# Kernel optimization log

Hardware: AMD Instinct MI355X
Metric: run time of the kernel (lower is better)

## Reference

```python
import jax, jax.numpy as jnp
import numpy as np

P = 256        # number of graph pairs
LMAX = 32      # max graph size (padded to LMAX+1 incl. virtual node)
F = 2048       # num_input_features
E = 256        # embedding_dim
INF = 10000.0


def _lengths():
    i = np.arange(P)
    len_s = 8 + (i % 25)
    len_t = 8 + ((7 * i + 3) % 25)
    return len_s.astype(np.int32), len_t.astype(np.int32)


def setup_inputs() -> dict:
    key = jax.random.key(0)
    ks = jax.random.split(key, 6)
    len_s_np, len_t_np = _lengths()
    Ns, Nt = int(len_s_np.sum()), int(len_t_np.sum())
    x_s = jax.random.normal(ks[0], (Ns, F), jnp.float32)
    x_t = jax.random.normal(ks[1], (Nt, F), jnp.float32)
    W1 = jax.random.normal(ks[2], (E, F), jnp.float32) / np.float32(np.sqrt(F))
    b1 = jnp.zeros((E,), jnp.float32)
    W2 = jax.random.normal(ks[3], (E, E), jnp.float32) / np.float32(np.sqrt(E))
    b2 = jnp.zeros((E,), jnp.float32)
    virtual_embedding = jax.random.uniform(ks[4], (F,), jnp.float32)
    return {"x_s": x_s, "x_t": x_t, "W1": W1, "b1": b1, "W2": W2, "b2": b2,
            "virtual_embedding": virtual_embedding,
            "len_s": jnp.asarray(len_s_np), "len_t": jnp.asarray(len_t_np)}


def _embed(x, W1, b1, W2, b2):
    # nn.Sequential(Linear, Dropout(eval=identity), ReLU, Linear, ReLU)
    h = jax.nn.relu(x @ W1.T + b1)
    return jax.nn.relu(h @ W2.T + b2)


def _safe_cdist(a, b):
    # a: [P,L,E], b: [P,L,E] -> [P,L,L] Euclidean, grad-safe at 0
    sq = (jnp.sum(a * a, -1)[:, :, None] + jnp.sum(b * b, -1)[:, None, :]
          - 2.0 * jnp.einsum('pid,pjd->pij', a, b))
    sq = jnp.maximum(sq, 0.0)
    pos = sq > 0
    return jnp.where(pos, jnp.sqrt(jnp.where(pos, sq, 1.0)), 0.0)


def _pad_embed(emb, virtual_e, lens):
    # ragged [N,E] -> padded [P,LMAX+1,E]; slot lens[p] (and beyond) = virtual
    pos = jnp.arange(LMAX + 1)
    off = jnp.cumsum(lens) - lens                       # exclusive prefix sum
    idx = off[:, None] + jnp.minimum(pos[None, :], lens[:, None] - 1)
    mask = pos[None, :] < lens[:, None]
    return jnp.where(mask[..., None], emb[idx], virtual_e[None, None, :])


def _edit_costs(x_s, x_t, W1, b1, W2, b2, virtual_embedding, len_s, len_t):
    emb_s = _embed(x_s, W1, b1, W2, b2)
    emb_t = _embed(x_t, W1, b1, W2, b2)
    ve = _embed(virtual_embedding[None, :], W1, b1, W2, b2)[0]
    A = _pad_embed(emb_s, ve, len_s)                    # [P,L+1,E]
    B = _pad_embed(emb_t, ve, len_t)
    d = _safe_cdist(A, B)                               # [P,L+1,L+1]
    pos = jnp.arange(LMAX + 1)
    valid = ((pos[None, :, None] <= len_s[:, None, None]) &
             (pos[None, None, :] <= len_t[:, None, None]))
    tot = jnp.sum(jnp.where(valid, d, 0.0), axis=(1, 2))
    scale = (len_s * len_t).astype(d.dtype) / tot
    return jnp.where(valid, d * scale[:, None, None], 0.0), valid


def _lap_jv(C):
    # Jonker-Volgenant / e-maxx Hungarian for square cost matrix; returns col of each row
    C = np.asarray(C, dtype=np.float64)
    n = C.shape[0]
    u = np.zeros(n + 1)
    v = np.zeros(n + 1)
    p = np.zeros(n + 1, dtype=np.int64)
    way = np.zeros(n + 1, dtype=np.int64)
    for i in range(1, n + 1):
        p[0] = i
        j0 = 0
        minv = np.full(n + 1, np.inf)
        used = np.zeros(n + 1, dtype=bool)
        while True:
            used[j0] = True
            i0 = p[j0]
            cur = C[i0 - 1, :] - u[i0] - v[1:]
            upd = (~used[1:]) & (cur < minv[1:])
            minv[1:][upd] = cur[upd]
            way[1:][upd] = j0
            masked = np.where(used[1:], np.inf, minv[1:])
            j1 = int(np.argmin(masked)) + 1
            delta = masked[j1 - 1]
            u[p[used]] += delta
            v[used] -= delta
            minv[1:][~used[1:]] -= delta
            j0 = j1
            if p[j0] == 0:
                break
        while j0:
            j1 = way[j0]
            p[j0] = p[j1]
            j0 = j1
    row_of_col = p[1:] - 1
    col_of_row = np.empty(n, dtype=np.int64)
    col_of_row[row_of_col] = np.arange(n)
    return col_of_row


def _lsape_align(ec, n, m):
    # LSAPE expansion identical to GEDModelHomology.lsape
    N = n + m
    C = np.zeros((N, N))
    C[:n, :m] = ec[:n, :m]
    C[n:, :m] = INF
    C[:n, m:] = INF
    C[np.arange(n, n + m), np.arange(m)] = ec[n, :m]
    C[np.arange(n), np.arange(m, m + n)] = ec[:n, m]
    C[~np.isfinite(C)] = INF
    p = _lap_jv(C)
    q = np.arange(N)
    align = np.zeros((n + 1, m + 1), dtype=np.int32)
    align[np.minimum(q, n), np.minimum(p, m)] = 1
    align[-1, -1] = 0
    return align


def _alignments(costs_np, len_s_np, len_t_np):
    out = np.zeros((costs_np.shape[0], LMAX + 1, LMAX + 1), dtype=np.int32)
    for pr in range(costs_np.shape[0]):
        n, m = int(len_s_np[pr]), int(len_t_np[pr])
        out[pr, :n + 1, :m + 1] = _lsape_align(costs_np[pr, :n + 1, :m + 1], n, m)
    return out


def reference(x_s, x_t, W1, b1, W2, b2, virtual_embedding, len_s, len_t):
    costs, _ = _edit_costs(x_s, x_t, W1, b1, W2, b2, virtual_embedding, len_s, len_t)
    aligns = jnp.asarray(_alignments(np.asarray(costs),
                                     np.asarray(len_s), np.asarray(len_t)))
    geds = (jnp.sum(aligns.astype(costs.dtype) * costs, axis=(1, 2))
            / (len_s + len_t).astype(costs.dtype))
    return aligns, costs, geds
```

## Files before the change

kernel.cpp:

```cpp
#include <hip/hip_runtime.h>
#include <math.h>

#define LMAXP1 33
#define EDIM   256
#define FBIG   3.0e38f

typedef _Float16 half8 __attribute__((ext_vector_type(8)));
typedef float    f32x4 __attribute__((ext_vector_type(4)));

__device__ inline unsigned pk2h(_Float16 a, _Float16 b) {
    union { _Float16 h[2]; unsigned u; } q; q.h[0] = a; q.h[1] = b; return q.u;
}

__global__ __launch_bounds__(256)
void k_convw(const float* __restrict__ W, unsigned* __restrict__ Wh,
             unsigned* __restrict__ Wl, int npairs, float scale) {
    const int stride = gridDim.x * blockDim.x;
    for (int i = blockIdx.x * blockDim.x + threadIdx.x; i < npairs; i += stride) {
        const float a0 = W[2*i] * scale, a1 = W[2*i+1] * scale;
        const _Float16 h0 = (_Float16)a0, h1 = (_Float16)a1;
        const _Float16 l0 = (_Float16)(a0 - (float)h0);
        const _Float16 l1 = (_Float16)(a1 - (float)h1);
        Wh[i] = pk2h(h0, h1); Wl[i] = pk2h(l0, l1);
    }
}

__global__ __launch_bounds__(256)
void k_norms(const unsigned* __restrict__ Eh, const unsigned* __restrict__ El,
             float* __restrict__ Norms, int Mtot) {
    const int row  = blockIdx.x * 4 + (threadIdx.x >> 6);
    const int lane = threadIdx.x & 63;
    if (row >= Mtot) return;
    const uint2 h2 = *(const uint2*)(Eh + (size_t)row * 128 + lane * 2);
    const uint2 l2 = *(const uint2*)(El + (size_t)row * 128 + lane * 2);
    union { unsigned u; _Float16 h[2]; } qh, ql;
    float s = 0.f;
    qh.u = h2.x; ql.u = l2.x;
    { const float x0 = (float)qh.h[0] + (float)ql.h[0];
      const float x1 = (float)qh.h[1] + (float)ql.h[1];
      s = fmaf(x0, x0, s); s = fmaf(x1, x1, s); }
    qh.u = h2.y; ql.u = l2.y;
    { const float x0 = (float)qh.h[0] + (float)ql.h[0];
      const float x1 = (float)qh.h[1] + (float)ql.h[1];
      s = fmaf(x0, x0, s); s = fmaf(x1, x1, s); }
    #pragma unroll
    for (int off = 32; off > 0; off >>= 1) s += __shfl_xor(s, off);
    if (lane == 0) Norms[row] = s;
}

#define ASTR 20
__global__ __launch_bounds__(256)
void k_gemm_splitk(const float* __restrict__ S0, int n0,
                   const float* __restrict__ S1, int n1,
                   const float* __restrict__ S2,
                   const unsigned* __restrict__ Wh, const unsigned* __restrict__ Wl,
                   float* __restrict__ Part, int Mtot, int K, int kchunk) {
    __shared__ alignas(16) unsigned AsH[64 * ASTR],  AsL[64 * ASTR];
    __shared__ alignas(16) unsigned BsH[128 * ASTR], BsL[128 * ASTR];
    const int tid = threadIdx.x;
    const int m0  = blockIdx.x * 64;
    const int nc0 = blockIdx.y * 128;
    const int ks  = blockIdx.z;
    const int kb  = ks * kchunk;
    const int ke  = (kb + kchunk < K) ? kb + kchunk : K;

    const int sar = tid >> 2, sak = (tid & 3) << 3;
    const int gr  = m0 + sar;
    const float* srow = nullptr;
    if (gr < n0)            srow = S0 + (size_t)gr * K;
    else if (gr < n0 + n1)  srow = S1 + (size_t)(gr - n0) * K;
    else if (gr < Mtot)     srow = S2;

    const int lane = tid & 63, wv = tid >> 6;
    const int wc = wv << 5;
    const int lr = lane & 15, lq = lane >> 4;

    f32x4 acc[4][2] = {};

    for (int k0 = kb; k0 < ke; k0 += 32) {
        {
            float x[8];
            if (srow) {
                const float4 f0 = *(const float4*)(srow + k0 + sak + 0);
                const float4 f1 = *(const float4*)(srow + k0 + sak + 4);
                x[0]=f0.x; x[1]=f0.y; x[2]=f0.z; x[3]=f0.w;
                x[4]=f1.x; x[5]=f1.y; x[6]=f1.z; x[7]=f1.w;
            } else {
                #pragma unroll
                for (int j = 0; j < 8; ++j) x[j] = 0.f;
            }
            unsigned uh[4], ul[4];
            #pragma unroll
            for (int j = 0; j < 4; ++j) {
                const _Float16 h0 = (_Float16)x[2*j],   h1 = (_Float16)x[2*j+1];
                const _Float16 l0 = (_Float16)(x[2*j]   - (float)h0);
                const _Float16 l1 = (_Float16)(x[2*j+1] - (float)h1);
                uh[j] = pk2h(h0, h1); ul[j] = pk2h(l0, l1);
            }
            *(uint4*)(AsH + sar * ASTR + (sak >> 1)) = make_uint4(uh[0],uh[1],uh[2],uh[3]);
            *(uint4*)(AsL + sar * ASTR + (sak >> 1)) = make_uint4(ul[0],ul[1],ul[2],ul[3]);
        }
        #pragma unroll
        for (int it = 0; it < 2; ++it) {
            const int idx = tid + it * 256;
            const int br = idx >> 2, bk = (idx & 3) << 3;
            const size_t uoff = (size_t)(nc0 + br) * (K >> 1) + ((k0 + bk) >> 1);
            *(uint4*)(BsH + br * ASTR + (bk >> 1)) = *(const uint4*)(Wh + uoff);
            *(uint4*)(BsL + br * ASTR + (bk >> 1)) = *(const uint4*)(Wl + uoff);
        }
        __syncthreads();

        half8 bhv[2], blv[2];
        #pragma unroll
        for (int ct = 0; ct < 2; ++ct) {
            const int br = wc + ct * 16 + lr;
            bhv[ct] = *(const half8*)((const char*)BsH + br * 80 + lq * 16);
            blv[ct] = *(const half8*)((const char*)BsL + br * 80 + lq * 16);
        }
        #pragma unroll
        for (int rt = 0; rt < 4; ++rt) {
            const int ar = rt * 16 + lr;
            const half8 ah = *(const half8*)((const char*)AsH + ar * 80 + lq * 16);
            const half8 al = *(const half8*)((const char*)AsL + ar * 80 + lq * 16);
            #pragma unroll
            for (int ct = 0; ct < 2; ++ct) {
                acc[rt][ct] = __builtin_amdgcn_mfma_f32_16x16x32_f16(ah, bhv[ct], acc[rt][ct], 0, 0, 0);
                acc[rt][ct] = __builtin_amdgcn_mfma_f32_16x16x32_f16(ah, blv[ct], acc[rt][ct], 0, 0, 0);
                acc[rt][ct] = __builtin_amdgcn_mfma_f32_16x16x32_f16(al, bhv[ct], acc[rt][ct], 0, 0, 0);
            }
        }
        __syncthreads();
    }

    float* pout = Part + (size_t)ks * ((size_t)Mtot * EDIM);
    const float sc = 1.0f / 1024.0f;
    #pragma unroll
    for (int rt = 0; rt < 4; ++rt) {
        #pragma unroll
        for (int r = 0; r < 4; ++r) {
            const int grr = m0 + rt * 16 + lq * 4 + r;
            if (grr >= Mtot) continue;
            #pragma unroll
            for (int ct = 0; ct < 2; ++ct)
                pout[(size_t)grr * EDIM + nc0 + wc + ct * 16 + lr] = acc[rt][ct][r] * sc;
        }
    }
}

__global__ __launch_bounds__(256)
void k_reduce_bias_relu(const float* __restrict__ Part,
                        const float* __restrict__ bias,
                        unsigned* __restrict__ Hh, unsigned* __restrict__ Hl,
                        int S, size_t MN4) {
    const size_t i = (size_t)blockIdx.x * blockDim.x + threadIdx.x;
    const size_t stride = (size_t)gridDim.x * blockDim.x;
    const size_t MN = MN4 * 4;
    for (size_t i4 = i; i4 < MN4; i4 += stride) {
        float4 s = ((const float4*)Part)[i4];
        for (int z = 1; z < S; ++z)
            { const float4 q = ((const float4*)(Part + (size_t)z * MN))[i4];
              s.x += q.x; s.y += q.y; s.z += q.z; s.w += q.w; }
        const float4 b = ((const float4*)bias)[i4 & 63];
        s.x = fmaxf(s.x + b.x, 0.f); s.y = fmaxf(s.y + b.y, 0.f);
        s.z = fmaxf(s.z + b.z, 0.f); s.w = fmaxf(s.w + b.w, 0.f);
        const _Float16 hx = (_Float16)s.x, hy = (_Float16)s.y;
        const _Float16 hz = (_Float16)s.z, hw = (_Float16)s.w;
        Hh[i4*2+0] = pk2h(hx, hy);
        Hh[i4*2+1] = pk2h(hz, hw);
        Hl[i4*2+0] = pk2h((_Float16)(s.x - (float)hx), (_Float16)(s.y - (float)hy));
        Hl[i4*2+1] = pk2h((_Float16)(s.z - (float)hz), (_Float16)(s.w - (float)hw));
    }
}

__global__ __launch_bounds__(256)
void k_gemm_f16(const unsigned* __restrict__ Ah, const unsigned* __restrict__ Al,
                const unsigned* __restrict__ Wh, const unsigned* __restrict__ Wl,
                const float* __restrict__ bias,
                unsigned* __restrict__ Eh, unsigned* __restrict__ El,
                int Mtot, int K) {
    __shared__ alignas(16) unsigned AsH[64 * ASTR],  AsL[64 * ASTR];
    __shared__ alignas(16) unsigned BsH[256 * ASTR], BsL[256 * ASTR];
    const int tid = threadIdx.x;
    const int m0  = blockIdx.x * 64;

    const int sar = tid >> 2, sak = (tid & 3) << 3;
    const int gr  = m0 + sar;
    const bool arow = (gr < Mtot);

    const int lane = tid & 63, wv = tid >> 6;
    const int wc = wv << 6;
    const int lr = lane & 15, lq = lane >> 4;

    f32x4 acc[4][4] = {};

    for (int k0 = 0; k0 < K; k0 += 32) {
        {
            uint4 vh = make_uint4(0,0,0,0), vl = vh;
            if (arow) {
                const size_t uoff = (size_t)gr * (K >> 1) + ((k0 + sak) >> 1);
                vh = *(const uint4*)(Ah + uoff);
                vl = *(const uint4*)(Al + uoff);
            }
            *(uint4*)(AsH + sar * ASTR + (sak >> 1)) = vh;
            *(uint4*)(AsL + sar * ASTR + (sak >> 1)) = vl;
        }
        #pragma unroll
        for (int it = 0; it < 4; ++it) {
            const int idx = tid + it * 256;
            const int br = idx >> 2, bk = (idx & 3) << 3;
            const size_t uoff = (size_t)br * (K >> 1) + ((k0 + bk) >> 1);
            *(uint4*)(BsH + br * ASTR + (bk >> 1)) = *(const uint4*)(Wh + uoff);
            *(uint4*)(BsL + br * ASTR + (bk >> 1)) = *(const uint4*)(Wl + uoff);
        }
        __syncthreads();

        half8 bhv[4], blv[4];
        #pragma unroll
        for (int ct = 0; ct < 4; ++ct) {
            const int br = wc + ct * 16 + lr;
            bhv[ct] = *(const half8*)((const char*)BsH + br * 80 + lq * 16);
            blv[ct] = *(const half8*)((const char*)BsL + br * 80 + lq * 16);
        }
        #pragma unroll
        for (int rt = 0; rt < 4; ++rt) {
            const int ar = rt * 16 + lr;
            const half8 ah = *(const half8*)((const char*)AsH + ar * 80 + lq * 16);
            const half8 al = *(const half8*)((const char*)AsL + ar * 80 + lq * 16);
            #pragma unroll
            for (int ct = 0; ct < 4; ++ct) {
                acc[rt][ct] = __builtin_amdgcn_mfma_f32_16x16x32_f16(ah, bhv[ct], acc[rt][ct], 0, 0, 0);
                acc[rt][ct] = __builtin_amdgcn_mfma_f32_16x16x32_f16(ah, blv[ct], acc[rt][ct], 0, 0, 0);
                acc[rt][ct] = __builtin_amdgcn_mfma_f32_16x16x32_f16(al, bhv[ct], acc[rt][ct], 0, 0, 0);
            }
        }
        __syncthreads();
    }

    _Float16* ph = (_Float16*)Eh;
    _Float16* pl = (_Float16*)El;
    const float sc = 1.0f / 1024.0f;
    #pragma unroll
    for (int rt = 0; rt < 4; ++rt) {
        #pragma unroll
        for (int r = 0; r < 4; ++r) {
            const int grr = m0 + rt * 16 + lq * 4 + r;
            if (grr >= Mtot) continue;
            #pragma unroll
            for (int ct = 0; ct < 4; ++ct) {
                const int gc = wc + ct * 16 + lr;
                const float vv = fmaxf(acc[rt][ct][r] * sc + bias[gc], 0.0f);
                const _Float16 hv = (_Float16)vv;
                ph[(size_t)grr * EDIM + gc] = hv;
                pl[(size_t)grr * EDIM + gc] = (_Float16)(vv - (float)hv);
            }
        }
    }
}

__global__ __launch_bounds__(256)
void k_embed_gemm(const float* __restrict__ S0, int n0,
                  const float* __restrict__ S1, int n1,
                  const float* __restrict__ S2,
                  const float* __restrict__ W, const float* __restrict__ bias,
                  float* __restrict__ C, int Mtot, int K) {
    __shared__ alignas(16) float As[16][68];
    __shared__ alignas(16) float Bs[16][68];
    const int tid  = threadIdx.x;
    const int tx   = tid & 15, ty = tid >> 4;
    const int m0   = blockIdx.x * 64, nc0 = blockIdx.y * 64;
    const int lrow = tid >> 2;
    const int lk4  = (tid & 3) << 2;

    const int gr = m0 + lrow;
    const float* srow = nullptr;
    if (gr < n0)            srow = S0 + (size_t)gr * K;
    else if (gr < n0 + n1)  srow = S1 + (size_t)(gr - n0) * K;
    else if (gr < Mtot)     srow = S2;
    const float* wrow = W + (size_t)(nc0 + lrow) * K;

    float acc[4][4] = {};
    for (int k0 = 0; k0 < K; k0 += 16) {
        float4 va = make_float4(0.f, 0.f, 0.f, 0.f);
        if (srow) va = *(const float4*)(srow + k0 + lk4);
        const float4 vb = *(const float4*)(wrow + k0 + lk4);
        As[lk4+0][lrow] = va.x; As[lk4+1][lrow] = va.y;
        As[lk4+2][lrow] = va.z; As[lk4+3][lrow] = va.w;
        Bs[lk4+0][lrow] = vb.x; Bs[lk4+1][lrow] = vb.y;
        Bs[lk4+2][lrow] = vb.z; Bs[lk4+3][lrow] = vb.w;
        __syncthreads();
        #pragma unroll
        for (int kk = 0; kk < 16; ++kk) {
            const float4 a4 = *(const float4*)&As[kk][ty << 2];
            const float4 b4 = *(const float4*)&Bs[kk][tx << 2];
            const float av[4] = {a4.x, a4.y, a4.z, a4.w};
            const float bv[4] = {b4.x, b4.y, b4.z, b4.w};
            #pragma unroll
            for (int i2 = 0; i2 < 4; ++i2)
                #pragma unroll
                for (int j2 = 0; j2 < 4; ++j2)
                    acc[i2][j2] = fmaf(av[i2], bv[j2], acc[i2][j2]);
        }
        __syncthreads();
    }
    #pragma unroll
    for (int i2 = 0; i2 < 4; ++i2) {
        const int grr = m0 + (ty << 2) + i2;
        if (grr >= Mtot) continue;
        #pragma unroll
        for (int j2 = 0; j2 < 4; ++j2) {
            const int gc = nc0 + (tx << 2) + j2;
            const float vv = acc[i2][j2] + bias[gc];
            C[(size_t)grr * EDIM + gc] = fmaxf(vv, 0.0f);
        }
    }
}

#define CSTR 36
__global__ __launch_bounds__(256)
void k_costs(const unsigned* __restrict__ Eh, const unsigned* __restrict__ El,
             const float* __restrict__ Norms,
             const int* __restrict__ len_s, const int* __restrict__ len_t,
             int Ns, int Nt, float* __restrict__ costs) {
    __shared__ alignas(16) unsigned Ah[34 * CSTR], Al[34 * CSTR];
    __shared__ alignas(16) unsigned Bh[34 * CSTR], Bl[34 * CSTR];
    __shared__ float dtile[LMAXP1 * LMAXP1];
    __shared__ float na[LMAXP1], nb[LMAXP1];
    __shared__ float red[256];
    __shared__ float s_scale;
    const int p = blockIdx.x, tid = threadIdx.x;
    const int n = len_s[p], m = len_t[p];
    int offs = 0, offt = 0;
    for (int j = 0; j < p; ++j) { offs += len_s[j]; offt += len_t[j]; }
    const int veRow = Ns + Nt;
    const int tbase = Ns + offt;

    const int lane = tid & 63, wv = tid >> 6;
    const int lr = lane & 15, lq = lane >> 4;

    if (tid <= n)                       na[tid] = Norms[(tid < n) ? offs + tid : veRow];
    else if (tid >= 64 && tid - 64 <= m) nb[tid - 64] = Norms[(tid - 64 < m) ? tbase + tid - 64 : veRow];

    f32x4 g0 = {}, g1 = {}, g2 = {};
    const int t0 = wv, t1 = wv + 4, t2 = wv + 8;

    for (int k0 = 0; k0 < EDIM; k0 += 64) {
        for (int idx = tid; idx < 34 * 16; idx += 256) {
            const int r = idx >> 4, c4 = idx & 15;
            const int rowA = (r < n) ? offs + r : ((r == n) ? veRow : -1);
            const int rowB = (r < m) ? tbase + r : ((r == m) ? veRow : -1);
            uint2 vah = make_uint2(0,0), val = vah, vbh = vah, vbl = vah;
            if (rowA >= 0) {
                const size_t uo_ = (size_t)rowA * 128 + (k0 >> 1) + c4 * 2;
                vah = *(const uint2*)(Eh + uo_); val = *(const uint2*)(El + uo_);
            }
            if (rowB >= 0) {
                const size_t uo_ = (size_t)rowB * 128 + (k0 >> 1) + c4 * 2;
                vbh = *(const uint2*)(Eh + uo_); vbl = *(const uint2*)(El + uo_);
            }
            const int uo = r * CSTR + c4 * 2;
            *(uint2*)(Ah + uo) = vah; *(uint2*)(Al + uo) = val;
            *(uint2*)(Bh + uo) = vbh; *(uint2*)(Bl + uo) = vbl;
        }
        __syncthreads();

        #pragma unroll
        for (int kf = 0; kf < 2; ++kf) {
#define GRAM_TILE(T, G) { \
            const int tr_ = (T) / 3, tc_ = (T) % 3;                              \
            const int ar_ = tr_ * 16 + lr, br_ = tc_ * 16 + lr;                  \
            const half8 ah = *(const half8*)((const char*)Ah + ar_*144 + kf*64 + lq*16); \
            const half8 al = *(const half8*)((const char*)Al + ar_*144 + kf*64 + lq*16); \
            const half8 bh = *(const half8*)((const char*)Bh + br_*144 + kf*64 + lq*16); \
            const half8 bl = *(const half8*)((const char*)Bl + br_*144 + kf*64 + lq*16); \
            G = __builtin_amdgcn_mfma_f32_16x16x32_f16(ah, bh, G, 0, 0, 0);      \
            G = __builtin_amdgcn_mfma_f32_16x16x32_f16(ah, bl, G, 0, 0, 0);      \
            G = __builtin_amdgcn_mfma_f32_16x16x32_f16(al, bh, G, 0, 0, 0); }
            GRAM_TILE(t0, g0)
            GRAM_TILE(t1, g1)
            if (wv == 0) GRAM_TILE(t2, g2)
#undef GRAM_TILE
        }
        __syncthreads();
    }

#define DTILE_OUT(T, G) { \
    const int tr_ = (T) / 3, tc_ = (T) % 3;                                      \
    _Pragma("unroll")                                                            \
    for (int r = 0; r < 4; ++r) {                                                \
        const int i_ = tr_ * 16 + lq * 4 + r, j_ = tc_ * 16 + lr;                \
        if (i_ <= n && j_ <= m) {                                                \
            const float sq = fmaxf(na[i_] + nb[j_] - 2.0f * G[r], 0.0f);         \
            dtile[i_ * LMAXP1 + j_] = (sq > 0.0f) ? sqrtf(sq) : 0.0f;            \
        } } }
    DTILE_OUT(t0, g0)
    DTILE_OUT(t1, g1)
    if (wv == 0) DTILE_OUT(t2, g2)
#undef DTILE_OUT
    __syncthreads();

    float lsum = 0.f;
    const int m1 = m + 1;
    const int cells = (n + 1) * m1;
    for (int c = tid; c < cells; c += 256) {
        const int i = c / m1, j = c - i * m1;
        lsum += dtile[i * LMAXP1 + j];
    }
    red[tid] = lsum;
    __syncthreads();
    for (int s = 128; s > 0; s >>= 1) {
        if (tid < s) red[tid] += red[tid + s];
        __syncthreads();
    }
    if (tid == 0) s_scale = (float)(n * m) / red[0];
    __syncthreads();
    const float scale = s_scale;
    for (int idx = tid; idx < LMAXP1 * LMAXP1; idx += 256) {
        const int i = idx / LMAXP1, j = idx - i * LMAXP1;
        const float v = (i <= n && j <= m) ? dtile[i * LMAXP1 + j] * scale : 0.0f;
        costs[(size_t)p * (LMAXP1 * LMAXP1) + idx] = v;
    }
}

__device__ inline int rdlane_i(int v, int l) { return __builtin_amdgcn_readlane(v, l); }
__device__ inline float rdlane_f(float v, int l) {
    return __int_as_float(__builtin_amdgcn_readlane(__float_as_int(v), l));
}
__device__ inline unsigned wave_umin64(unsigned x) {
#define DPPMINU(ctrl) { unsigned t_ = (unsigned)__builtin_amdgcn_update_dpp(  \
        (int)x, (int)x, (ctrl), 0xf, 0xf, false);                             \
        x = (t_ < x) ? t_ : x; }
    DPPMINU(0xB1)
    DPPMINU(0x4E)
    DPPMINU(0x141)
    DPPMINU(0x140)
    DPPMINU(0x142)
    DPPMINU(0x143)
#undef DPPMINU
    return (unsigned)__builtin_amdgcn_readlane((int)x, 63);
}

__global__ __launch_bounds__(64)
void k_lap(const float* __restrict__ costs, const int* __restrict__ len_s,
           const int* __restrict__ len_t, float* __restrict__ aligns,
           float* __restrict__ geds) {
    __shared__ float ec[LMAXP1 * LMAXP1];
    __shared__ float Ms[33 * 64];
    const int p = blockIdx.x, lane = threadIdx.x;
    const int n = len_s[p], m = len_t[p];
    const float* cp = costs + (size_t)p * (LMAXP1 * LMAXP1);
    for (int idx = lane; idx < LMAXP1 * LMAXP1; idx += 64) ec[idx] = cp[idx];
    __syncthreads();

    const bool swp = (n > m);
    const int R  = swp ? n : m;
    const int S_ = swp ? m : n;
    const bool vec = (lane >= 1 && lane <= R);

    for (int r = 1; r <= R; ++r) {
        float cv = FBIG;
        const int i0b = r - 1, j0b = lane - 1;
        if (vec) {
            if (!swp) {
                const float ins = ec[n * LMAXP1 + j0b];
                cv = (i0b < S_)
                   ? fminf(ec[i0b * LMAXP1 + j0b], ec[i0b * LMAXP1 + m] + ins)
                   : ins;
            } else {
                const float ins = ec[j0b * LMAXP1 + m];
                cv = (i0b < S_)
                   ? fminf(ec[j0b * LMAXP1 + i0b], ec[n * LMAXP1 + i0b] + ins)
                   : ins;
            }
        }
        Ms[(r << 6) + lane] = cv;
    }
    __syncthreads();

    float v_l = 0.0f;
    int amin_l = 0;
    if (vec) {
        float best = FBIG;
        for (int r = 1; r <= R; ++r) {
            const float c = Ms[(r << 6) + lane];
            if (c < best) { best = c; amin_l = r; }
        }
        v_l = best;
    }
    int p_l = 0;
    unsigned long long rowfree = ((1ull << R) - 1ull) << 1;
    for (int j = 1; j <= R; ++j) {
        const int ai = rdlane_i(amin_l, j);
        if ((rowfree >> ai) & 1ull) {
            if (lane == j) p_l = ai;
            rowfree &= ~(1ull << ai);
        }
    }

    float ucol = 0.0f;
    {
        unsigned long long q = rowfree;
        int pops = 0;
        const int cap = 3 * R;
        while (q && pops < cap) {
            const int i = __ffsll(q) - 1;
            q &= ~(1ull << i);
            ++pops;
            const float rc = vec ? fmaxf(Ms[(i << 6) + lane] - v_l, 0.0f) : FBIG;
            const unsigned key = (__float_as_uint(rc) & ~63u) | (unsigned)lane;
            const unsigned k1 = wave_umin64(key);
            int j1 = (int)(k1 & 63u);
            const float min1 = rdlane_f(rc, j1);
            const unsigned key2 = (lane == j1) ? 0xFFFFFFFFu : key;
            const unsigned k2 = wave_umin64(key2);
            const float min2 = rdlane_f(rc, (int)(k2 & 63u));
            int owner = rdlane_i(p_l, j1);
            const bool strict = (min1 < min2);
            if (!strict) {
                const unsigned long long ball =
                    __ballot(vec && (rc == min1) && (p_l == 0));
                if (ball == 0ull) continue;
                j1 = __ffsll(ball) - 1;
                j1 = __builtin_amdgcn_readfirstlane(j1);
                owner = 0;
            }
            if (lane == j1) {
                p_l = i; ucol = min2;
                if (strict) v_l -= (min2 - min1);
            }
            rowfree &= ~(1ull << i);
            if (owner != 0) { rowfree |= (1ull << owner); q |= (1ull << owner); }
        }
    }

    float minv_l = FBIG;
    int way_l = 0;

    for (int i = 1; i <= R; ++i) {
        if (!((rowfree >> i) & 1ull)) continue;
        if (lane == 0) { p_l = i; ucol = 0.0f; }
        minv_l = FBIG;
        int used_l = 0;
        int j0 = 0, i0 = i;
        float u_i0 = 0.0f;
        while (true) {
            if (lane == j0) used_l = 1;
            const float cur = Ms[(i0 << 6) + lane] - u_i0 - v_l;
            const bool unused = vec && !used_l;
            if (unused && cur < minv_l) { minv_l = cur; way_l = j0; }
            const float mval = unused ? fmaxf(minv_l, 0.0f) : FBIG;
            const unsigned key = (__float_as_uint(mval) & ~63u) | (unsigned)lane;
            const unsigned kmin = wave_umin64(key);
            const int j1 = (int)(kmin & 63u);
            const float delta = rdlane_f(minv_l, j1);
            if (used_l) { ucol += delta; v_l -= delta; }
            if (unused) minv_l -= delta;
            j0 = j1;
            i0 = rdlane_i(p_l, j1);
            u_i0 = rdlane_f(ucol, j1);
            if (i0 == 0) break;
        }
        int jj = j0;
        while (jj != 0) {
            const int   j1a = rdlane_i(way_l, jj);
            const int   pn  = rdlane_i(p_l, j1a);
            const float un  = rdlane_f(ucol, j1a);
            if (lane == jj) { p_l = pn; ucol = un; }
            jj = j1a;
        }
    }

    float* ap = aligns + (size_t)p * (LMAXP1 * LMAXP1);
    for (int idx = lane; idx < LMAXP1 * LMAXP1; idx += 64) ap[idx] = 0.0f;
    __syncthreads();
    float gedv = 0.0f;
    if (vec) {
        const int i0b = p_l - 1;
        const int j0b = lane - 1;
        if (!swp) {
            if (i0b < S_) {
                const float sub = ec[i0b * LMAXP1 + j0b];
                const float alt = ec[i0b * LMAXP1 + m] + ec[n * LMAXP1 + j0b];
                if (sub <= alt) { ap[i0b * LMAXP1 + j0b] = 1.0f; gedv = sub; }
                else { ap[i0b * LMAXP1 + m] = 1.0f;
                       ap[n * LMAXP1 + j0b] = 1.0f;
                       gedv = alt; }
            } else {
                ap[n * LMAXP1 + j0b] = 1.0f;
                gedv = ec[n * LMAXP1 + j0b];
            }
        } else {
            if (i0b < S_) {
                const float sub = ec[j0b * LMAXP1 + i0b];
                const float alt = ec[n * LMAXP1 + i0b] + ec[j0b * LMAXP1 + m];
                if (sub <= alt) { ap[j0b * LMAXP1 + i0b] = 1.0f; gedv = sub; }
                else { ap[n * LMAXP1 + i0b] = 1.0f;
                       ap[j0b * LMAXP1 + m] = 1.0f;
                       gedv = alt; }
            } else {
                ap[j0b * LMAXP1 + m] = 1.0f;
                gedv = ec[j0b * LMAXP1 + m];
            }
        }
    }
    #pragma unroll
    for (int off = 32; off > 0; off >>= 1) gedv += __shfl_xor(gedv, off);
    if (lane == 0) geds[p] = gedv / (float)(n + m);
}

extern "C" void kernel_launch(void* const* d_in, const int* in_sizes, int n_in,
                              void* d_out, int out_size, void* d_ws, size_t ws_size,
                              hipStream_t stream) {
    const float* x_s = (const float*)d_in[0];
    const float* x_t = (const float*)d_in[1];
    const float* W1  = (const float*)d_in[2];
    const float* b1  = (const float*)d_in[3];
    const float* W2  = (const float*)d_in[4];
    const float* b2  = (const float*)d_in[5];
    const float* ve  = (const float*)d_in[6];
    const int* len_s = (const int*)d_in[7];
    const int* len_t = (const int*)d_in[8];
    const int P    = in_sizes[7];
    const int Ns   = in_sizes[0] / 2048;
    const int Nt   = in_sizes[1] / 2048;
    const int Mtot = Ns + Nt + 1;
    const size_t MN  = (size_t)Mtot * EDIM;

    float* out_aligns = (float*)d_out;
    float* out_costs  = out_aligns + (size_t)P * LMAXP1 * LMAXP1;
    float* out_geds   = out_costs  + (size_t)P * LMAXP1 * LMAXP1;

    const dim3 b256(256);
    const int gx64 = (Mtot + 63) / 64;
    const int gnorm = (Mtot + 3) / 4;

    const size_t fixed = MN + 10240 + 2 * 262144 + 2 * 32768;
    int S = 0;
    if (ws_size >= (4 * MN + fixed) * sizeof(float)) S = 4;
    else if (ws_size >= (2 * MN + fixed) * sizeof(float)) S = 2;

    if (S > 0) {
        float* Part = (float*)d_ws;
        unsigned* Eh  = (unsigned*)Part;
        unsigned* El  = Eh + MN / 2;
        unsigned* Hh  = (unsigned*)(Part + (size_t)S * MN);
        unsigned* Hl  = Hh + MN / 2;
        float* Norms  = (float*)(Hl + MN / 2);
        unsigned* W1h = (unsigned*)(Norms + 10240);
        unsigned* W1l = W1h + 262144;
        unsigned* W2h = W1l + 262144;
        unsigned* W2l = W2h + 32768;

        k_convw<<<dim3(1024), b256, 0, stream>>>(W1, W1h, W1l, 262144, 1024.0f);
        k_convw<<<dim3(128),  b256, 0, stream>>>(W2, W2h, W2l, 32768, 1024.0f);

        k_gemm_splitk<<<dim3(gx64, 2, S), b256, 0, stream>>>(
            x_s, Ns, x_t, Nt, ve, W1h, W1l, Part, Mtot, 2048, 2048 / S);

        const size_t MN4 = MN / 4;
        const int rblocks = (int)((MN4 + 255) / 256) < 2048
                          ? (int)((MN4 + 255) / 256) : 2048;
        k_reduce_bias_relu<<<dim3(rblocks), b256, 0, stream>>>(Part, b1, Hh, Hl, S, MN4);

        k_gemm_f16<<<dim3(gx64), b256, 0, stream>>>(Hh, Hl, W2h, W2l, b2, Eh, El, Mtot, 256);
        k_norms<<<dim3(gnorm), b256, 0, stream>>>(Eh, El, Norms, Mtot);

        k_costs<<<dim3(P), b256, 0, stream>>>(Eh, El, Norms, len_s, len_t, Ns, Nt, out_costs);
        k_lap<<<dim3(P), dim3(64), 0, stream>>>(out_costs, len_s, len_t, out_aligns, out_geds);
    } else {
        float* H   = (float*)d_ws;
        float* Emb = H + MN;
        unsigned* Eh = (unsigned*)(Emb + MN);
        unsigned* El = Eh + MN / 2;
        float* Norms = (float*)(El + MN / 2);
        k_embed_gemm<<<dim3(gx64, 4), b256, 0, stream>>>(
            x_s, Ns, x_t, Nt, ve, W1, b1, H, Mtot, 2048);
        k_embed_gemm<<<dim3(gx64, 4), b256, 0, stream>>>(
            H, Mtot, nullptr, 0, nullptr, W2, b2, Emb, Mtot, 256);
        k_convw<<<dim3(1024), b256, 0, stream>>>(Emb, Eh, El, (int)(MN / 2), 1.0f);
        k_norms<<<dim3(gnorm), b256, 0, stream>>>(Eh, El, Norms, Mtot);
        k_costs<<<dim3(P), b256, 0, stream>>>(Eh, El, Norms, len_s, len_t, Ns, Nt, out_costs);
        k_lap<<<dim3(P), dim3(64), 0, stream>>>(out_costs, len_s, len_t, out_aligns, out_geds);
    }
}
```

Before: 168.7 us.

## Double-buffer A tile in split-K GEMM and load W fragments directly from global

The split-K GEMM now double-buffers the converted fp16 hi/lo A tile in shared memory. It prefetches the next K slice of the input rows into registers while the MFMAs for the current slice run, which removes one barrier per iteration. The weight tile is no longer staged through shared memory: each lane loads its half8 B fragments straight from the pre-converted global weight arrays. This cuts LDS traffic and synchronisation, but it relies on cache hits for weight reuse across row tiles and may cause uncoalesced global loads.

```diff
diff --git a/kernel.cpp b/kernel.cpp
--- a/kernel.cpp
+++ b/kernel.cpp
@@ -55,8 +55,7 @@
                    const float* __restrict__ S2,
                    const unsigned* __restrict__ Wh, const unsigned* __restrict__ Wl,
                    float* __restrict__ Part, int Mtot, int K, int kchunk) {
-    __shared__ alignas(16) unsigned AsH[64 * ASTR],  AsL[64 * ASTR];
-    __shared__ alignas(16) unsigned BsH[128 * ASTR], BsL[128 * ASTR];
+    __shared__ alignas(16) unsigned AsH[2][64 * ASTR], AsL[2][64 * ASTR];
     const int tid = threadIdx.x;
     const int m0  = blockIdx.x * 64;
     const int nc0 = blockIdx.y * 128;
@@ -75,59 +74,73 @@
     const int wc = wv << 5;
     const int lr = lane & 15, lq = lane >> 4;
 
+    const size_t browu = (size_t)(nc0 + wc + lr) * (size_t)(K >> 1);
+    const size_t bct   = (size_t)16 * (size_t)(K >> 1);
+
     f32x4 acc[4][2] = {};
 
-    for (int k0 = kb; k0 < ke; k0 += 32) {
-        {
-            float x[8];
-            if (srow) {
-                const float4 f0 = *(const float4*)(srow + k0 + sak + 0);
-                const float4 f1 = *(const float4*)(srow + k0 + sak + 4);
-                x[0]=f0.x; x[1]=f0.y; x[2]=f0.z; x[3]=f0.w;
-                x[4]=f1.x; x[5]=f1.y; x[6]=f1.z; x[7]=f1.w;
-            } else {
-                #pragma unroll
-                for (int j = 0; j < 8; ++j) x[j] = 0.f;
-            }
-            unsigned uh[4], ul[4];
-            #pragma unroll
-            for (int j = 0; j < 4; ++j) {
-                const _Float16 h0 = (_Float16)x[2*j],   h1 = (_Float16)x[2*j+1];
-                const _Float16 l0 = (_Float16)(x[2*j]   - (float)h0);
-                const _Float16 l1 = (_Float16)(x[2*j+1] - (float)h1);
-                uh[j] = pk2h(h0, h1); ul[j] = pk2h(l0, l1);
-            }
-            *(uint4*)(AsH + sar * ASTR + (sak >> 1)) = make_uint4(uh[0],uh[1],uh[2],uh[3]);
-            *(uint4*)(AsL + sar * ASTR + (sak >> 1)) = make_uint4(ul[0],ul[1],ul[2],ul[3]);
-        }
-        #pragma unroll
-        for (int it = 0; it < 2; ++it) {
-            const int idx = tid + it * 256;
-            const int br = idx >> 2, bk = (idx & 3) << 3;
-            const size_t uoff = (size_t)(nc0 + br) * (K >> 1) + ((k0 + bk) >> 1);
-            *(uint4*)(BsH + br * ASTR + (bk >> 1)) = *(const uint4*)(Wh + uoff);
-            *(uint4*)(BsL + br * ASTR + (bk >> 1)) = *(const uint4*)(Wl + uoff);
-        }
-        __syncthreads();
-
+    float xa[8];
+    #pragma unroll
+    for (int j = 0; j < 8; ++j) xa[j] = 0.f;
+    if (srow) {
+        const float4 f0 = *(const float4*)(srow + kb + sak + 0);
+        const float4 f1 = *(const float4*)(srow + kb + sak + 4);
+        xa[0]=f0.x; xa[1]=f0.y; xa[2]=f0.z; xa[3]=f0.w;
+        xa[4]=f1.x; xa[5]=f1.y; xa[6]=f1.z; xa[7]=f1.w;
+    }
+    {
+        unsigned uh[4], ul[4];
+        #pragma unroll
+        for (int j = 0; j < 4; ++j) {
+            const _Float16 h0 = (_Float16)xa[2*j],   h1 = (_Float16)xa[2*j+1];
+            const _Float16 l0 = (_Float16)(xa[2*j]   - (float)h0);
+            const _Float16 l1 = (_Float16)(xa[2*j+1] - (float)h1);
+            uh[j] = pk2h(h0, h1); ul[j] = pk2h(l0, l1);
+        }
+        *(uint4*)(AsH[0] + sar * ASTR + (sak >> 1)) = make_uint4(uh[0],uh[1],uh[2],uh[3]);
+        *(uint4*)(AsL[0] + sar * ASTR + (sak >> 1)) = make_uint4(ul[0],ul[1],ul[2],ul[3]);
+    }
+    __syncthreads();
+
+    int buf = 0;
+    for (int k0 = kb; k0 < ke; k0 += 32, buf ^= 1) {
+        const bool hasNext = (k0 + 32 < ke);
+        if (hasNext && srow) {
+            const float4 f0 = *(const float4*)(srow + k0 + 32 + sak + 0);
+            const float4 f1 = *(const float4*)(srow + k0 + 32 + sak + 4);
+            xa[0]=f0.x; xa[1]=f0.y; xa[2]=f0.z; xa[3]=f0.w;
+            xa[4]=f1.x; xa[5]=f1.y; xa[6]=f1.z; xa[7]=f1.w;
+        }
+        const size_t bko = (size_t)(k0 >> 1) + (size_t)(lq << 2);
         half8 bhv[2], blv[2];
         #pragma unroll
         for (int ct = 0; ct < 2; ++ct) {
-            const int br = wc + ct * 16 + lr;
-            bhv[ct] = *(const half8*)((const char*)BsH + br * 80 + lq * 16);
-            blv[ct] = *(const half8*)((const char*)BsL + br * 80 + lq * 16);
+            bhv[ct] = *(const half8*)(Wh + browu + (size_t)ct * bct + bko);
+            blv[ct] = *(const half8*)(Wl + browu + (size_t)ct * bct + bko);
         }
         #pragma unroll
         for (int rt = 0; rt < 4; ++rt) {
             const int ar = rt * 16 + lr;
-            const half8 ah = *(const half8*)((const char*)AsH + ar * 80 + lq * 16);
-            const half8 al = *(const half8*)((const char*)AsL + ar * 80 + lq * 16);
+            const half8 ah = *(const half8*)((const char*)AsH[buf] + ar * 80 + lq * 16);
+            const half8 al = *(const half8*)((const char*)AsL[buf] + ar * 80 + lq * 16);
             #pragma unroll
             for (int ct = 0; ct < 2; ++ct) {
                 acc[rt][ct] = __builtin_amdgcn_mfma_f32_16x16x32_f16(ah, bhv[ct], acc[rt][ct], 0, 0, 0);
                 acc[rt][ct] = __builtin_amdgcn_mfma_f32_16x16x32_f16(ah, blv[ct], acc[rt][ct], 0, 0, 0);
                 acc[rt][ct] = __builtin_amdgcn_mfma_f32_16x16x32_f16(al, bhv[ct], acc[rt][ct], 0, 0, 0);
             }
+        }
+        if (hasNext) {
+            unsigned uh[4], ul[4];
+            #pragma unroll
+            for (int j = 0; j < 4; ++j) {
+                const _Float16 h0 = (_Float16)xa[2*j],   h1 = (_Float16)xa[2*j+1];
+                const _Float16 l0 = (_Float16)(xa[2*j]   - (float)h0);
+                const _Float16 l1 = (_Float16)(xa[2*j+1] - (float)h1);
+                uh[j] = pk2h(h0, h1); ul[j] = pk2h(l0, l1);
+            }
+            *(uint4*)(AsH[buf ^ 1] + sar * ASTR + (sak >> 1)) = make_uint4(uh[0],uh[1],uh[2],uh[3]);
+            *(uint4*)(AsL[buf ^ 1] + sar * ASTR + (sak >> 1)) = make_uint4(ul[0],ul[1],ul[2],ul[3]);
         }
         __syncthreads();
     }
```

New measurement: 173.2 us. 2.7% more time.
